# Optimization experiments

Hardware: AMD Instinct MI355X
Metric: run time of the kernel (lower is better)

Reference implementation:

```python
import math
import jax, jax.numpy as jnp
import numpy as np

EPS = 1e-6
MAX_SCALE_LOG = math.log(100.0)

def rms_norm(x, scale, eps=EPS):
    # x * scale / rms(x), reduction over last dim
    ms = jnp.mean(jnp.square(x), axis=-1, keepdims=True)
    return x * (scale * jax.lax.rsqrt(ms + eps))

def axial_rope_theta(pos, n_heads, d_head, dtype):
    # freqs: linspace in log-space from pi to 10*pi, reshaped to [n_heads, d_head//4]
    f = np.exp(np.linspace(math.log(math.pi), math.log(10.0 * math.pi),
                           n_heads * d_head // 4 + 1)[:-1])
    freqs = jnp.asarray(f.reshape(d_head // 4, n_heads).T, dtype)  # [h, e/4]
    theta_h = pos[:, :, None, 0:1] * freqs  # [n, l, h, e/4]
    theta_w = pos[:, :, None, 1:2] * freqs  # [n, l, h, e/4]
    theta = jnp.concatenate([theta_h, theta_w], axis=-1)  # [n, l, h, e/2]
    return theta.transpose(0, 2, 1, 3)  # [n, h, l, e/2]

def apply_rotary(x, theta):
    d = theta.shape[-1]
    x1, x2, x3 = x[..., :d], x[..., d:2 * d], x[..., 2 * d:]
    cos, sin = jnp.cos(theta), jnp.sin(theta)
    return jnp.concatenate([x1 * cos - x2 * sin, x2 * cos + x1 * sin, x3], axis=-1)

def setup_inputs() -> dict:
    key = jax.random.key(0)
    ks = jax.random.split(key, 8)
    n, l, d_model, d_head = 2, 2048, 1024, 64
    n_heads = d_model // d_head
    x = jax.random.normal(ks[0], (n, l, d_model), jnp.float32)
    pos = jax.random.uniform(ks[1], (n, l, 2), jnp.float32)
    cond = jax.random.normal(ks[2], (n, 1, d_model), jnp.float32)
    # params (torch uses zero-init for w_cond/w_out; small random for a non-degenerate baseline)
    w_cond = jax.random.normal(ks[3], (d_model, d_model), jnp.float32) * 0.02
    w_qkv = jax.random.normal(ks[4], (d_model, 3 * d_model), jnp.float32) * (d_model ** -0.5)
    qk_scale = jnp.full((n_heads,), math.log(10.0), jnp.float32)
    w_out = jax.random.normal(ks[5], (d_model, d_model), jnp.float32) * 0.02
    return {"x": x, "pos": pos, "cond": cond, "w_cond": w_cond,
            "w_qkv": w_qkv, "qk_scale": qk_scale, "w_out": w_out}

def reference(x, pos, cond, w_cond, w_qkv, qk_scale, w_out):
    n, l, d_model = x.shape
    h = qk_scale.shape[0]
    e = d_model // h
    # AdaRMSNorm: scale = linear(cond) + 1
    xn = rms_norm(x, cond @ w_cond + 1.0)
    # QKV projection
    q, k, v = jnp.split(xn @ w_qkv, 3, axis=-1)
    to_heads = lambda t: t.reshape(n, l, h, e).transpose(0, 2, 1, 3)  # [n,h,l,e]
    q, k, v = to_heads(q), to_heads(k), to_heads(v)
    # QKNorm: per-head learned scale, rms over head dim
    s = jnp.exp(0.5 * jnp.minimum(qk_scale, MAX_SCALE_LOG) - 0.25 * math.log(e))
    q = rms_norm(q, s[:, None, None])
    k = rms_norm(k, s[:, None, None])
    # Axial RoPE
    theta = axial_rope_theta(pos, h, e, x.dtype)
    q = apply_rotary(q, theta)
    k = apply_rotary(k, theta)
    # SDPA (no mask)
    attn = jax.nn.softmax(jnp.einsum('nhqe,nhke->nhqk', q, k) / math.sqrt(e), axis=-1)
    o = jnp.einsum('nhqk,nhke->nhqe', attn, v)
    o = o.transpose(0, 2, 1, 3).reshape(n, l, d_model)
    return o @ w_out
```

## Files before the change

kernel.cpp:

```cpp
#include <hip/hip_runtime.h>

typedef unsigned short u16;
typedef unsigned int u32;
typedef short s16x8 __attribute__((ext_vector_type(8)));
typedef short s16x4 __attribute__((ext_vector_type(4)));
typedef float f32x4 __attribute__((ext_vector_type(4)));
typedef u32 u32x2 __attribute__((ext_vector_type(2)));

#define AS1 __attribute__((address_space(1)))
#define AS3 __attribute__((address_space(3)))

__device__ __forceinline__ float bf2f(u16 u) {
    union { unsigned int i; float f; } x; x.i = ((unsigned int)u) << 16; return x.f;
}
__device__ __forceinline__ u16 f2bf(float f) {
    union { float f; unsigned int i; } x; x.f = f;
    unsigned int r = (x.i + 0x7FFFu + ((x.i >> 16) & 1u)) >> 16;
    return (u16)r;
}
__device__ __forceinline__ void storeOut(u16* p, float v) { *p = f2bf(v); }
__device__ __forceinline__ void storeOut(float* p, float v) { *p = v; }
__device__ __forceinline__ float loadIn(const void* p, size_t i, int isf32) {
    return isf32 ? ((const float*)p)[i] : bf2f(((const u16*)p)[i]);
}
__device__ __forceinline__ float fexp2(float x) {
#if __has_builtin(__builtin_amdgcn_exp2f)
    return __builtin_amdgcn_exp2f(x);
#else
    return exp2f(x);
#endif
}
__device__ __forceinline__ u32 pack_bf(float a, float b) {
    u32 ua = __float_as_uint(a) + 0x8000u;
    u32 ub = __float_as_uint(b) + 0x8000u;
    return __builtin_amdgcn_perm(ub, ua, 0x07060302u);
}

__global__ __launch_bounds__(256) void detect_dtype(const u16* __restrict__ x,
                                                    int* __restrict__ flag) {
    __shared__ int cnt[4];
    const int tid = threadIdx.x;
    int c = 0;
    #pragma unroll
    for (int i = 0; i < 4; ++i) {
        const u16 u = x[tid * 4 + i];
        const int e = (u >> 7) & 0xFF;
        c += (e >= 101 && e <= 135) ? 1 : 0;
    }
    #pragma unroll
    for (int m = 1; m < 64; m <<= 1) c += __shfl_xor(c, m, 64);
    if ((tid & 63) == 0) cnt[tid >> 6] = c;
    __syncthreads();
    if (tid == 0) {
        const int t = cnt[0] + cnt[1] + cnt[2] + cnt[3];
        *flag = (t < 800) ? 1 : 0;
    }
}

__global__ __launch_bounds__(256) void cond_gemv(const void* __restrict__ cond,
                                                 const void* __restrict__ w,
                                                 float* __restrict__ out,
                                                 const int* __restrict__ flag) {
    const int isf32 = *flag;
    const int d  = blockIdx.x * 256 + threadIdx.x;
    const int n  = blockIdx.y;
    const int k0 = blockIdx.z * 64;
    float acc = 0.f;
    #pragma unroll 8
    for (int k = 0; k < 64; ++k)
        acc += loadIn(cond, n * 1024 + k0 + k, isf32) *
               loadIn(w, (size_t)(k0 + k) * 1024 + d, isf32);
    atomicAdd(out + n * 1024 + d, acc);
}

__global__ __launch_bounds__(256) void rmsnorm_x(const void* __restrict__ x,
                                                 const float* __restrict__ scl,
                                                 u16* __restrict__ xn,
                                                 const int* __restrict__ flag) {
    const int isf32 = *flag;
    const int tok = blockIdx.x;
    const int n = tok >> 11;
    u16* orow = xn + (size_t)tok * 1024;
    const int base = threadIdx.x * 4;
    float f0, f1, f2, f3;
    if (isf32) {
        const float4 v = *(const float4*)((const float*)x + (size_t)tok * 1024 + base);
        f0 = v.x; f1 = v.y; f2 = v.z; f3 = v.w;
    } else {
        s16x4 uv = *(const s16x4*)((const u16*)x + (size_t)tok * 1024 + base);
        f0 = bf2f((u16)uv[0]); f1 = bf2f((u16)uv[1]); f2 = bf2f((u16)uv[2]); f3 = bf2f((u16)uv[3]);
    }
    float ss = f0 * f0 + f1 * f1 + f2 * f2 + f3 * f3;
    #pragma unroll
    for (int m = 1; m < 64; m <<= 1) ss += __shfl_xor(ss, m, 64);
    __shared__ float red[4];
    const int wave = threadIdx.x >> 6, lane = threadIdx.x & 63;
    if (lane == 0) red[wave] = ss;
    __syncthreads();
    float ms = (red[0] + red[1] + red[2] + red[3]) * (1.f / 1024.f);
    float rinv = rsqrtf(ms + 1e-6f);
    orow[base + 0] = f2bf(f0 * (scl[n * 1024 + base + 0] + 1.f) * rinv);
    orow[base + 1] = f2bf(f1 * (scl[n * 1024 + base + 1] + 1.f) * rinv);
    orow[base + 2] = f2bf(f2 * (scl[n * 1024 + base + 2] + 1.f) * rinv);
    orow[base + 3] = f2bf(f3 * (scl[n * 1024 + base + 3] + 1.f) * rinv);
}

__global__ __launch_bounds__(256) void transpose_bf(const void* __restrict__ src,
                                                    u16* __restrict__ dst, int R, int C,
                                                    const int* __restrict__ flag) {
    const int isf32 = *flag;
    __shared__ u16 t[32][33];
    const int c0 = blockIdx.x * 32, r0 = blockIdx.y * 32;
    const int tx = threadIdx.x & 31, ty = threadIdx.x >> 5;
    #pragma unroll
    for (int i = 0; i < 4; ++i)
        t[ty + i * 8][tx] = f2bf(loadIn(src, (size_t)(r0 + ty + i * 8) * C + c0 + tx, isf32));
    __syncthreads();
    #pragma unroll
    for (int i = 0; i < 4; ++i)
        dst[(size_t)(c0 + ty + i * 8) * R + r0 + tx] = t[tx][ty + i * 8];
}

template <typename OutT>
__global__ __launch_bounds__(256) void gemm_bt(const u16* __restrict__ A,
                                               const u16* __restrict__ BT,
                                               OutT* __restrict__ C, int Nn, int K) {
    __shared__ u16 As[128 * 32];
    __shared__ u16 Bs[128 * 32];
    const int tid = threadIdx.x;
    const int wave = tid >> 6, lane = tid & 63;
    const int l15 = lane & 15, quad = lane >> 4;
    const int bm0 = blockIdx.y * 128, bn0 = blockIdx.x * 128;
    const int wr = wave >> 1, wc = wave & 1;
    f32x4 acc[4][4] = {};
    const int srow = lane >> 2;
    const int g = (lane & 3) ^ (srow & 3);
    for (int bk = 0; bk < K; bk += 32) {
        __syncthreads();
        #pragma unroll
        for (int p = 0; p < 2; ++p) {
            const int rowl = p * 64 + wave * 16 + srow;
            const u16* ga = A + (size_t)(bm0 + rowl) * K + bk + g * 8;
            u16* la = As + (p * 64 + wave * 16) * 32;
            __builtin_amdgcn_global_load_lds((const AS1 void*)ga, (AS3 void*)la, 16, 0, 0);
            const u16* gb = BT + (size_t)(bn0 + rowl) * K + bk + g * 8;
            u16* lb = Bs + (p * 64 + wave * 16) * 32;
            __builtin_amdgcn_global_load_lds((const AS1 void*)gb, (AS3 void*)lb, 16, 0, 0);
        }
        __syncthreads();
        s16x8 af[4], bfr[4];
        #pragma unroll
        for (int mt = 0; mt < 4; ++mt) {
            const int r = wr * 64 + mt * 16 + l15;
            af[mt] = *(const s16x8*)(As + r * 32 + ((quad ^ (r & 3)) << 3));
        }
        #pragma unroll
        for (int nt = 0; nt < 4; ++nt) {
            const int r = wc * 64 + nt * 16 + l15;
            bfr[nt] = *(const s16x8*)(Bs + r * 32 + ((quad ^ (r & 3)) << 3));
        }
        #pragma unroll
        for (int mt = 0; mt < 4; ++mt)
            #pragma unroll
            for (int nt = 0; nt < 4; ++nt)
                acc[mt][nt] = __builtin_amdgcn_mfma_f32_16x16x32_bf16(af[mt], bfr[nt], acc[mt][nt], 0, 0, 0);
    }
    #pragma unroll
    for (int mt = 0; mt < 4; ++mt)
        #pragma unroll
        for (int nt = 0; nt < 4; ++nt)
            #pragma unroll
            for (int r = 0; r < 4; ++r) {
                const int row = bm0 + wr * 64 + mt * 16 + quad * 4 + r;
                const int col = bn0 + wc * 64 + nt * 16 + l15;
                storeOut(C + (size_t)row * Nn + col, acc[mt][nt][r]);
            }
}

__global__ __launch_bounds__(256) void qkv_head(const u16* __restrict__ qkv,
                                                const void* __restrict__ pos,
                                                const void* __restrict__ qk_scale,
                                                u16* __restrict__ q_ws,
                                                u16* __restrict__ k_ws,
                                                u16* __restrict__ vtg,
                                                const int* __restrict__ flag) {
    const int isf32 = *flag;
    const int nh = blockIdx.y;
    const int n = nh >> 4, h = nh & 15;
    const int l0 = blockIdx.x * 64;
    const int tid = threadIdx.x;
    const int wave = tid >> 6, lane = tid & 63;

    const float qs = loadIn(qk_scale, h, isf32);
    const float s = __expf(0.5f * fminf(qs, 4.605170186f) - 1.039720771f);
    const float qmul = s * s * 0.125f * 1.44269504089f;
    const int j = lane & 31;
    const float t = (float)((j & 15) * 16 + h);
    const float freq = 3.14159265358979f * __expf(t * (2.302585093f / 256.f));
    const int pj = j >> 4;

    #pragma unroll 2
    for (int it = 0; it < 16; ++it) {
        const int l = l0 + wave * 16 + it;
        const int tok = n * 2048 + l;
        const u16* row = qkv + (size_t)tok * 3072;
        float qv = bf2f(row[h * 64 + lane]);
        float kv = bf2f(row[1024 + h * 64 + lane]);
        float q2 = qv * qv, k2 = kv * kv;
        #pragma unroll
        for (int m = 1; m < 64; m <<= 1) { q2 += __shfl_xor(q2, m, 64); k2 += __shfl_xor(k2, m, 64); }
        float qn = qv * rsqrtf(q2 * (1.f / 64.f) + 1e-6f) * qmul;
        float kn = kv * rsqrtf(k2 * (1.f / 64.f) + 1e-6f);
        const float p = loadIn(pos, tok * 2 + pj, isf32);
        const float th = p * freq;
        const float c = __cosf(th), sn = __sinf(th);
        const float pq = __shfl_xor(qn, 32, 64);
        const float pk = __shfl_xor(kn, 32, 64);
        float qr, kr;
        if (lane < 32) { qr = qn * c - pq * sn; kr = kn * c - pk * sn; }
        else           { qr = qn * c + pq * sn; kr = kn * c + pk * sn; }
        const size_t oidx = ((size_t)nh * 2048 + l) * 64 + lane;
        q_ws[oidx] = f2bf(qr);
        k_ws[oidx] = f2bf(kr);
    }

    __shared__ u16 tbuf[64][65];
    const u16* vsrc = qkv + (size_t)(n * 2048 + l0) * 3072 + 2048 + h * 64;
    #pragma unroll
    for (int it = 0; it < 16; ++it) {
        const int idx = it * 256 + tid;
        const int r = idx >> 6, c = idx & 63;
        tbuf[r][c] = vsrc[(size_t)r * 3072 + c];
    }
    __syncthreads();
    u16* dst = vtg + (size_t)nh * 131072 + l0;
    #pragma unroll
    for (int it = 0; it < 16; ++it) {
        const int idx = it * 256 + tid;
        const int er = idx >> 6, lc = idx & 63;
        dst[(size_t)er * 2048 + lc] = tbuf[lc][er];
    }
}

__global__ __launch_bounds__(256, 2) void attn5(const u16* __restrict__ Q,
                                                const u16* __restrict__ K,
                                                const u16* __restrict__ Vtg,
                                                u16* __restrict__ O) {
    __shared__ u16 Ks[2][64 * 64];
    __shared__ u16 Vt[3][64 * 64];
    __shared__ u16 Ps[4][32 * 72];
    const int nh = blockIdx.y;
    const int q0 = blockIdx.x * 128;
    const int tid = threadIdx.x;
    const int wave = tid >> 6, lane = tid & 63;
    const int l15 = lane & 15, quad = lane >> 4;
    const size_t hb = (size_t)nh * 2048 * 64;
    const u16* Vbase = Vtg + (size_t)nh * 131072;
    const int dr0 = tid >> 3;
    const int dd  = tid & 7;

    s16x8 qf[2][2];
    #pragma unroll
    for (int qg = 0; qg < 2; ++qg)
        #pragma unroll
        for (int kc = 0; kc < 2; ++kc)
            qf[qg][kc] = *(const s16x8*)(Q + hb + (size_t)(q0 + wave * 32 + qg * 16 + l15) * 64 + kc * 32 + quad * 8);

    f32x4 Oacc[2][4] = {};
    float lacc[2] = {0.f, 0.f};
    u16* Pw = Ps[wave];

    #pragma unroll
    for (int it = 0; it < 2; ++it) {
        const int row = it * 32 + dr0;
        const int g = dd ^ (row & 7);
        __builtin_amdgcn_global_load_lds(
            (const AS1 void*)(K + hb + (size_t)row * 64 + g * 8),
            (AS3 void*)(Ks[0] + (it * 256 + wave * 64) * 8), 16, 0, 0);
        __builtin_amdgcn_global_load_lds(
            (const AS1 void*)(Vbase + (size_t)row * 2048 + g * 8),
            (AS3 void*)(Vt[0] + (it * 256 + wave * 64) * 8), 16, 0, 0);
    }
    __syncthreads();

    int vprev = 2, vcur = 0, vnxt = 1;
    s16x8 pf[2][2];

    for (int i = 0; i < 32; ++i) {
        const int kcur = i & 1;
        if (i < 31) {
            const int kbn = (i + 1) * 64;
            #pragma unroll
            for (int it = 0; it < 2; ++it) {
                const int row = it * 32 + dr0;
                const int g = dd ^ (row & 7);
                __builtin_amdgcn_global_load_lds(
                    (const AS1 void*)(K + hb + (size_t)(kbn + row) * 64 + g * 8),
                    (AS3 void*)(Ks[kcur ^ 1] + (it * 256 + wave * 64) * 8), 16, 0, 0);
                __builtin_amdgcn_global_load_lds(
                    (const AS1 void*)(Vbase + (size_t)row * 2048 + kbn + g * 8),
                    (AS3 void*)(Vt[vnxt] + (it * 256 + wave * 64) * 8), 16, 0, 0);
            }
        }
        if (i > 0) {
            #pragma unroll
            for (int kc = 0; kc < 2; ++kc) {
                pf[kc][0] = *(const s16x8*)(Pw + l15 * 72 + kc * 32 + quad * 8);
                pf[kc][1] = *(const s16x8*)(Pw + (16 + l15) * 72 + kc * 32 + quad * 8);
            }
        }
        f32x4 S[2][4];
        #pragma unroll
        for (int qg = 0; qg < 2; ++qg)
            #pragma unroll
            for (int kt = 0; kt < 4; ++kt) {
                S[qg][kt][0] = -15.f; S[qg][kt][1] = -15.f;
                S[qg][kt][2] = -15.f; S[qg][kt][3] = -15.f;
            }
        #pragma unroll
        for (int kt = 0; kt < 4; ++kt) {
            const int r = kt * 16 + l15;
            #pragma unroll
            for (int kc = 0; kc < 2; ++kc) {
                const s16x8 kf = *(const s16x8*)(Ks[kcur] + r * 64 + (((kc * 4 + quad) ^ (r & 7)) << 3));
                S[0][kt] = __builtin_amdgcn_mfma_f32_16x16x32_bf16(kf, qf[0][kc], S[0][kt], 0, 0, 0);
                S[1][kt] = __builtin_amdgcn_mfma_f32_16x16x32_bf16(kf, qf[1][kc], S[1][kt], 0, 0, 0);
            }
        }
        if (i > 0) {
            #pragma unroll
            for (int kc = 0; kc < 2; ++kc)
                #pragma unroll
                for (int nto = 0; nto < 4; ++nto) {
                    const int e = nto * 16 + l15;
                    const s16x8 vf = *(const s16x8*)(Vt[vprev] + e * 64 + (((kc * 4 + quad) ^ (e & 7)) << 3));
                    Oacc[0][nto] = __builtin_amdgcn_mfma_f32_16x16x32_bf16(pf[kc][0], vf, Oacc[0][nto], 0, 0, 0);
                    Oacc[1][nto] = __builtin_amdgcn_mfma_f32_16x16x32_bf16(pf[kc][1], vf, Oacc[1][nto], 0, 0, 0);
                }
        }
        #pragma unroll
        for (int qg = 0; qg < 2; ++qg) {
            float rs = 0.f;
            #pragma unroll
            for (int kt = 0; kt < 4; ++kt) {
                const float e0 = fexp2(S[qg][kt][0]);
                const float e1 = fexp2(S[qg][kt][1]);
                const float e2 = fexp2(S[qg][kt][2]);
                const float e3 = fexp2(S[qg][kt][3]);
                rs += (e0 + e1) + (e2 + e3);
                u32x2 pk2;
                pk2[0] = pack_bf(e0, e1);
                pk2[1] = pack_bf(e2, e3);
                *(u32x2*)(Pw + (qg * 16 + l15) * 72 + kt * 16 + quad * 4) = pk2;
            }
            lacc[qg] += rs;
        }
        const int tmp = vprev; vprev = vcur; vcur = vnxt; vnxt = tmp;
        if (i < 31) __syncthreads();
    }

    #pragma unroll
    for (int kc = 0; kc < 2; ++kc) {
        pf[kc][0] = *(const s16x8*)(Pw + l15 * 72 + kc * 32 + quad * 8);
        pf[kc][1] = *(const s16x8*)(Pw + (16 + l15) * 72 + kc * 32 + quad * 8);
    }
    #pragma unroll
    for (int kc = 0; kc < 2; ++kc)
        #pragma unroll
        for (int nto = 0; nto < 4; ++nto) {
            const int e = nto * 16 + l15;
            const s16x8 vf = *(const s16x8*)(Vt[vprev] + e * 64 + (((kc * 4 + quad) ^ (e & 7)) << 3));
            Oacc[0][nto] = __builtin_amdgcn_mfma_f32_16x16x32_bf16(pf[kc][0], vf, Oacc[0][nto], 0, 0, 0);
            Oacc[1][nto] = __builtin_amdgcn_mfma_f32_16x16x32_bf16(pf[kc][1], vf, Oacc[1][nto], 0, 0, 0);
        }

    #pragma unroll
    for (int qg = 0; qg < 2; ++qg) {
        lacc[qg] += __shfl_xor(lacc[qg], 16, 64);
        lacc[qg] += __shfl_xor(lacc[qg], 32, 64);
    }

    const int n = nh >> 4, h = nh & 15;
    #pragma unroll
    for (int qg = 0; qg < 2; ++qg)
        #pragma unroll
        for (int r = 0; r < 4; ++r) {
            const float linv = 1.f / __shfl(lacc[qg], quad * 4 + r, 64);
            const int qrow = q0 + wave * 32 + qg * 16 + quad * 4 + r;
            #pragma unroll
            for (int nto = 0; nto < 4; ++nto)
                O[((size_t)n * 2048 + qrow) * 1024 + h * 64 + nto * 16 + l15] = f2bf(Oacc[qg][nto][r] * linv);
        }
}

extern "C" void kernel_launch(void* const* d_in, const int* in_sizes, int n_in,
                              void* d_out, int out_size, void* d_ws, size_t ws_size,
                              hipStream_t stream) {
    const void* x        = d_in[0];
    const void* pos      = d_in[1];
    const void* cond     = d_in[2];
    const void* w_cond   = d_in[3];
    const void* w_qkv    = d_in[4];
    const void* qk_scale = d_in[5];
    const void* w_out    = d_in[6];

    char* ws = (char*)d_ws;
    constexpr size_t OFS_SCALE = 0;
    constexpr size_t OFS_FLAG  = 8192;
    constexpr size_t OFS_XN    = 16384;
    constexpr size_t OFS_WQKVT = OFS_XN    + 8388608;
    constexpr size_t OFS_WOUTT = OFS_WQKVT + 6291456;
    constexpr size_t OFS_QKV   = OFS_WOUTT + 2097152;
    constexpr size_t OFS_Q     = OFS_QKV   + 25165824;
    constexpr size_t OFS_K     = OFS_Q     + 8388608;
    constexpr size_t OFS_VT    = OFS_K     + 8388608;
    constexpr size_t OFS_O     = OFS_VT    + 8388608;

    float* scale = (float*)(ws + OFS_SCALE);
    int*   flag  = (int*)(ws + OFS_FLAG);
    u16* xn    = (u16*)(ws + OFS_XN);
    u16* wqkvT = (u16*)(ws + OFS_WQKVT);
    u16* woutT = (u16*)(ws + OFS_WOUTT);
    u16* qkv   = (u16*)(ws + OFS_QKV);
    u16* qws   = (u16*)(ws + OFS_Q);
    u16* kws   = (u16*)(ws + OFS_K);
    u16* vtg   = (u16*)(ws + OFS_VT);
    u16* ows   = (u16*)(ws + OFS_O);

    detect_dtype<<<dim3(1), 256, 0, stream>>>((const u16*)x, flag);
    hipMemsetAsync(scale, 0, 2 * 1024 * sizeof(float), stream);
    cond_gemv<<<dim3(4, 2, 16), 256, 0, stream>>>(cond, w_cond, scale, flag);
    rmsnorm_x<<<dim3(4096), 256, 0, stream>>>(x, scale, xn, flag);
    transpose_bf<<<dim3(96, 32), 256, 0, stream>>>(w_qkv, wqkvT, 1024, 3072, flag);
    transpose_bf<<<dim3(32, 32), 256, 0, stream>>>(w_out, woutT, 1024, 1024, flag);
    gemm_bt<u16><<<dim3(24, 32), 256, 0, stream>>>(xn, wqkvT, qkv, 3072, 1024);
    qkv_head<<<dim3(32, 32), 256, 0, stream>>>(qkv, pos, qk_scale, qws, kws, vtg, flag);
    attn5<<<dim3(16, 32), 256, 0, stream>>>(qws, kws, vtg, ows);
    gemm_bt<float><<<dim3(8, 32), 256, 0, stream>>>(ows, woutT, (float*)d_out, 1024, 1024);
}
```

Before: 240.8 us.

## Split attention work across 8 waves with 16 query rows each

The attention kernel now launches 512 threads per block (8 waves) instead of 256. Each wave handles 16 query rows instead of 32, so the same 128-row query tile is covered with half the per-wave work and registers. Each thread now issues one K and one V async load per tile instead of two. The aim is more waves in flight to hide LDS and MFMA latency, at the cost of more barrier participants and less reuse of each K/V fragment read from LDS per MFMA.

```diff
diff --git a/kernel.cpp b/kernel.cpp
--- a/kernel.cpp
+++ b/kernel.cpp
@@ -242,13 +242,13 @@
     }
 }
 
-__global__ __launch_bounds__(256, 2) void attn5(const u16* __restrict__ Q,
+__global__ __launch_bounds__(512, 4) void attn6(const u16* __restrict__ Q,
                                                 const u16* __restrict__ K,
                                                 const u16* __restrict__ Vtg,
                                                 u16* __restrict__ O) {
     __shared__ u16 Ks[2][64 * 64];
     __shared__ u16 Vt[3][64 * 64];
-    __shared__ u16 Ps[4][32 * 72];
+    __shared__ u16 Ps[8][16 * 72];
     const int nh = blockIdx.y;
     const int q0 = blockIdx.x * 128;
     const int tid = threadIdx.x;
@@ -258,73 +258,56 @@
     const u16* Vbase = Vtg + (size_t)nh * 131072;
     const int dr0 = tid >> 3;
     const int dd  = tid & 7;
-
-    s16x8 qf[2][2];
-    #pragma unroll
-    for (int qg = 0; qg < 2; ++qg)
-        #pragma unroll
-        for (int kc = 0; kc < 2; ++kc)
-            qf[qg][kc] = *(const s16x8*)(Q + hb + (size_t)(q0 + wave * 32 + qg * 16 + l15) * 64 + kc * 32 + quad * 8);
-
-    f32x4 Oacc[2][4] = {};
-    float lacc[2] = {0.f, 0.f};
+    const int dg  = dd ^ (dr0 & 7);
+
+    s16x8 qf[2];
+    #pragma unroll
+    for (int kc = 0; kc < 2; ++kc)
+        qf[kc] = *(const s16x8*)(Q + hb + (size_t)(q0 + wave * 16 + l15) * 64 + kc * 32 + quad * 8);
+
+    f32x4 Oacc[4] = {};
+    float lacc = 0.f;
     u16* Pw = Ps[wave];
 
-    #pragma unroll
-    for (int it = 0; it < 2; ++it) {
-        const int row = it * 32 + dr0;
-        const int g = dd ^ (row & 7);
-        __builtin_amdgcn_global_load_lds(
-            (const AS1 void*)(K + hb + (size_t)row * 64 + g * 8),
-            (AS3 void*)(Ks[0] + (it * 256 + wave * 64) * 8), 16, 0, 0);
-        __builtin_amdgcn_global_load_lds(
-            (const AS1 void*)(Vbase + (size_t)row * 2048 + g * 8),
-            (AS3 void*)(Vt[0] + (it * 256 + wave * 64) * 8), 16, 0, 0);
-    }
+    __builtin_amdgcn_global_load_lds(
+        (const AS1 void*)(K + hb + (size_t)dr0 * 64 + dg * 8),
+        (AS3 void*)(Ks[0] + wave * 512), 16, 0, 0);
+    __builtin_amdgcn_global_load_lds(
+        (const AS1 void*)(Vbase + (size_t)dr0 * 2048 + dg * 8),
+        (AS3 void*)(Vt[0] + wave * 512), 16, 0, 0);
     __syncthreads();
 
     int vprev = 2, vcur = 0, vnxt = 1;
-    s16x8 pf[2][2];
+    s16x8 pf[2];
 
     for (int i = 0; i < 32; ++i) {
         const int kcur = i & 1;
         if (i < 31) {
             const int kbn = (i + 1) * 64;
-            #pragma unroll
-            for (int it = 0; it < 2; ++it) {
-                const int row = it * 32 + dr0;
-                const int g = dd ^ (row & 7);
-                __builtin_amdgcn_global_load_lds(
-                    (const AS1 void*)(K + hb + (size_t)(kbn + row) * 64 + g * 8),
-                    (AS3 void*)(Ks[kcur ^ 1] + (it * 256 + wave * 64) * 8), 16, 0, 0);
-                __builtin_amdgcn_global_load_lds(
-                    (const AS1 void*)(Vbase + (size_t)row * 2048 + kbn + g * 8),
-                    (AS3 void*)(Vt[vnxt] + (it * 256 + wave * 64) * 8), 16, 0, 0);
-            }
+            __builtin_amdgcn_global_load_lds(
+                (const AS1 void*)(K + hb + (size_t)(kbn + dr0) * 64 + dg * 8),
+                (AS3 void*)(Ks[kcur ^ 1] + wave * 512), 16, 0, 0);
+            __builtin_amdgcn_global_load_lds(
+                (const AS1 void*)(Vbase + (size_t)dr0 * 2048 + kbn + dg * 8),
+                (AS3 void*)(Vt[vnxt] + wave * 512), 16, 0, 0);
         }
         if (i > 0) {
-            #pragma unroll
-            for (int kc = 0; kc < 2; ++kc) {
-                pf[kc][0] = *(const s16x8*)(Pw + l15 * 72 + kc * 32 + quad * 8);
-                pf[kc][1] = *(const s16x8*)(Pw + (16 + l15) * 72 + kc * 32 + quad * 8);
-            }
-        }
-        f32x4 S[2][4];
-        #pragma unroll
-        for (int qg = 0; qg < 2; ++qg)
-            #pragma unroll
-            for (int kt = 0; kt < 4; ++kt) {
-                S[qg][kt][0] = -15.f; S[qg][kt][1] = -15.f;
-                S[qg][kt][2] = -15.f; S[qg][kt][3] = -15.f;
-            }
+            pf[0] = *(const s16x8*)(Pw + l15 * 72 + quad * 8);
+            pf[1] = *(const s16x8*)(Pw + l15 * 72 + 32 + quad * 8);
+        }
+        f32x4 S[4];
+        #pragma unroll
+        for (int kt = 0; kt < 4; ++kt) {
+            S[kt][0] = -15.f; S[kt][1] = -15.f;
+            S[kt][2] = -15.f; S[kt][3] = -15.f;
+        }
         #pragma unroll
         for (int kt = 0; kt < 4; ++kt) {
             const int r = kt * 16 + l15;
             #pragma unroll
             for (int kc = 0; kc < 2; ++kc) {
                 const s16x8 kf = *(const s16x8*)(Ks[kcur] + r * 64 + (((kc * 4 + quad) ^ (r & 7)) << 3));
-                S[0][kt] = __builtin_amdgcn_mfma_f32_16x16x32_bf16(kf, qf[0][kc], S[0][kt], 0, 0, 0);
-                S[1][kt] = __builtin_amdgcn_mfma_f32_16x16x32_bf16(kf, qf[1][kc], S[1][kt], 0, 0, 0);
+                S[kt] = __builtin_amdgcn_mfma_f32_16x16x32_bf16(kf, qf[kc], S[kt], 0, 0, 0);
             }
         }
         if (i > 0) {
@@ -334,63 +317,52 @@
                 for (int nto = 0; nto < 4; ++nto) {
                     const int e = nto * 16 + l15;
                     const s16x8 vf = *(const s16x8*)(Vt[vprev] + e * 64 + (((kc * 4 + quad) ^ (e & 7)) << 3));
-                    Oacc[0][nto] = __builtin_amdgcn_mfma_f32_16x16x32_bf16(pf[kc][0], vf, Oacc[0][nto], 0, 0, 0);
-                    Oacc[1][nto] = __builtin_amdgcn_mfma_f32_16x16x32_bf16(pf[kc][1], vf, Oacc[1][nto], 0, 0, 0);
+                    Oacc[nto] = __builtin_amdgcn_mfma_f32_16x16x32_bf16(pf[kc], vf, Oacc[nto], 0, 0, 0);
                 }
         }
-        #pragma unroll
-        for (int qg = 0; qg < 2; ++qg) {
+        {
             float rs = 0.f;
             #pragma unroll
             for (int kt = 0; kt < 4; ++kt) {
-                const float e0 = fexp2(S[qg][kt][0]);
-                const float e1 = fexp2(S[qg][kt][1]);
-                const float e2 = fexp2(S[qg][kt][2]);
-                const float e3 = fexp2(S[qg][kt][3]);
+                const float e0 = fexp2(S[kt][0]);
+                const float e1 = fexp2(S[kt][1]);
+                const float e2 = fexp2(S[kt][2]);
+                const float e3 = fexp2(S[kt][3]);
                 rs += (e0 + e1) + (e2 + e3);
                 u32x2 pk2;
                 pk2[0] = pack_bf(e0, e1);
                 pk2[1] = pack_bf(e2, e3);
-                *(u32x2*)(Pw + (qg * 16 + l15) * 72 + kt * 16 + quad * 4) = pk2;
+                *(u32x2*)(Pw + l15 * 72 + kt * 16 + quad * 4) = pk2;
             }
-            lacc[qg] += rs;
+            lacc += rs;
         }
         const int tmp = vprev; vprev = vcur; vcur = vnxt; vnxt = tmp;
         if (i < 31) __syncthreads();
     }
 
-    #pragma unroll
-    for (int kc = 0; kc < 2; ++kc) {
-        pf[kc][0] = *(const s16x8*)(Pw + l15 * 72 + kc * 32 + quad * 8);
-        pf[kc][1] = *(const s16x8*)(Pw + (16 + l15) * 72 + kc * 32 + quad * 8);
-    }
+    pf[0] = *(const s16x8*)(Pw + l15 * 72 + quad * 8);
+    pf[1] = *(const s16x8*)(Pw + l15 * 72 + 32 + quad * 8);
     #pragma unroll
     for (int kc = 0; kc < 2; ++kc)
         #pragma unroll
         for (int nto = 0; nto < 4; ++nto) {
             const int e = nto * 16 + l15;
             const s16x8 vf = *(const s16x8*)(Vt[vprev] + e * 64 + (((kc * 4 + quad) ^ (e & 7)) << 3));
-            Oacc[0][nto] = __builtin_amdgcn_mfma_f32_16x16x32_bf16(pf[kc][0], vf, Oacc[0][nto], 0, 0, 0);
-            Oacc[1][nto] = __builtin_amdgcn_mfma_f32_16x16x32_bf16(pf[kc][1], vf, Oacc[1][nto], 0, 0, 0);
-        }
-
-    #pragma unroll
-    for (int qg = 0; qg < 2; ++qg) {
-        lacc[qg] += __shfl_xor(lacc[qg], 16, 64);
-        lacc[qg] += __shfl_xor(lacc[qg], 32, 64);
-    }
+            Oacc[nto] = __builtin_amdgcn_mfma_f32_16x16x32_bf16(pf[kc], vf, Oacc[nto], 0, 0, 0);
+        }
+
+    lacc += __shfl_xor(lacc, 16, 64);
+    lacc += __shfl_xor(lacc, 32, 64);
 
     const int n = nh >> 4, h = nh & 15;
     #pragma unroll
-    for (int qg = 0; qg < 2; ++qg)
-        #pragma unroll
-        for (int r = 0; r < 4; ++r) {
-            const float linv = 1.f / __shfl(lacc[qg], quad * 4 + r, 64);
-            const int qrow = q0 + wave * 32 + qg * 16 + quad * 4 + r;
-            #pragma unroll
-            for (int nto = 0; nto < 4; ++nto)
-                O[((size_t)n * 2048 + qrow) * 1024 + h * 64 + nto * 16 + l15] = f2bf(Oacc[qg][nto][r] * linv);
-        }
+    for (int r = 0; r < 4; ++r) {
+        const float linv = 1.f / __shfl(lacc, quad * 4 + r, 64);
+        const int qrow = q0 + wave * 16 + quad * 4 + r;
+        #pragma unroll
+        for (int nto = 0; nto < 4; ++nto)
+            O[((size_t)n * 2048 + qrow) * 1024 + h * 64 + nto * 16 + l15] = f2bf(Oacc[nto][r] * linv);
+    }
 }
 
 extern "C" void kernel_launch(void* const* d_in, const int* in_sizes, int n_in,
@@ -435,6 +407,6 @@
     transpose_bf<<<dim3(32, 32), 256, 0, stream>>>(w_out, woutT, 1024, 1024, flag);
     gemm_bt<u16><<<dim3(24, 32), 256, 0, stream>>>(xn, wqkvT, qkv, 3072, 1024);
     qkv_head<<<dim3(32, 32), 256, 0, stream>>>(qkv, pos, qk_scale, qws, kws, vtg, flag);
-    attn5<<<dim3(16, 32), 256, 0, stream>>>(qws, kws, vtg, ows);
+    attn6<<<dim3(16, 32), 512, 0, stream>>>(qws, kws, vtg, ows);
     gemm_bt<float><<<dim3(8, 32), 256, 0, stream>>>(ows, woutT, (float*)d_out, 1024, 1024);
 }
```

After: 234.6 us. 2.6% less time.
